# Kernel tuning notes

Measured on AMD Instinct MI355X. Metric: run time of the kernel, lower is better.

Reference implementation:

```python
import jax, jax.numpy as jnp
import numpy as np

N_NODES = 100000
N_EDGES = 1600000
D_IN = 128
D_HID = 128
D_OUT = 64


def setup_inputs() -> dict:
    key = jax.random.key(0)
    ks = jax.random.split(key, 8)
    x = jax.random.normal(ks[0], (N_NODES, D_IN), dtype=jnp.float32)
    edge_index = jax.random.randint(ks[1], (2, N_EDGES), 0, N_NODES, dtype=jnp.int64)
    s1 = 1.0 / np.sqrt(D_IN)
    s2 = 1.0 / np.sqrt(D_HID)
    W1 = jax.random.uniform(ks[2], (D_IN, D_HID), jnp.float32, -s1, s1)
    b1 = jnp.zeros((D_HID,), jnp.float32)
    W2 = jax.random.uniform(ks[3], (D_HID, D_HID), jnp.float32, -s2, s2)
    b2 = jnp.zeros((D_HID,), jnp.float32)
    fc_W = jax.random.uniform(ks[4], (D_HID, D_OUT), jnp.float32, -s2, s2)
    fc_b = jax.random.uniform(ks[5], (D_OUT,), jnp.float32, -s2, s2)
    return {"x": x, "edge_index": edge_index, "W1": W1, "b1": b1,
            "W2": W2, "b2": b2, "fc_W": fc_W, "fc_b": fc_b}


def _gcn_norm(edge_index, n_nodes):
    # add self-loops, compute symmetric normalization D^{-1/2} A D^{-1/2}
    loops = jnp.arange(n_nodes, dtype=edge_index.dtype)
    src = jnp.concatenate([edge_index[0], loops])  # [E+N]
    dst = jnp.concatenate([edge_index[1], loops])
    ones = jnp.ones(src.shape[0], jnp.float32)
    deg = jax.ops.segment_sum(ones, dst, num_segments=n_nodes)  # [N]
    dinv = 1.0 / jnp.sqrt(deg)  # deg >= 1 thanks to self-loops
    norm = dinv[src] * dinv[dst]  # [E+N]
    return src, dst, norm


def _gcn_conv(x, W, b, src, dst, norm, n_nodes):
    h = x @ W                                  # [N, d]
    msg = h[src] * norm[:, None]               # gather + scale, [E+N, d]
    out = jax.ops.segment_sum(msg, dst, num_segments=n_nodes)  # scatter-add
    return out + b


def reference(x, edge_index, W1, b1, W2, b2, fc_W, fc_b):
    n = x.shape[0]
    src, dst, norm = _gcn_norm(edge_index, n)
    h = jax.nn.relu(_gcn_conv(x, W1, b1, src, dst, norm, n))
    # dropout is identity in inference mode
    h = jax.nn.relu(_gcn_conv(h, W2, b2, src, dst, norm, n))
    return h @ fc_W + fc_b
```

## Files before the change

kernel.cpp:

```cpp
#include <hip/hip_runtime.h>

typedef __attribute__((ext_vector_type(8))) short bf16x8;
typedef __attribute__((ext_vector_type(4))) float f32x4;
typedef __attribute__((ext_vector_type(2))) float f32x2;

__device__ __forceinline__ unsigned short f2bf(float x) {
  union { float f; unsigned u; } v; v.f = x;
  return (unsigned short)((v.u + 0x7fffu + ((v.u >> 16) & 1u)) >> 16);
}


__global__ __launch_bounds__(256) void bhist_k(const int* __restrict__ dst,
                                               int* __restrict__ bcnt, int E, int B) {
  __shared__ int h[512];
  for (int i = threadIdx.x; i < B; i += 256) h[i] = 0;
  __syncthreads();
  for (int e = blockIdx.x * 256 + threadIdx.x; e < E; e += gridDim.x * 256)
    atomicAdd(&h[dst[e] >> 8], 1);
  __syncthreads();
  for (int i = threadIdx.x; i < B; i += 256)
    if (h[i]) atomicAdd(&bcnt[i * 16], h[i]);
}

__global__ __launch_bounds__(256) void bin_k(const int* __restrict__ src,
                                             const int* __restrict__ dst,
                                             const int* __restrict__ bcnt,
                                             int* __restrict__ bfill,
                                             unsigned* __restrict__ ebuf, int E, int B) {
  __shared__ int hist[512];
  __shared__ int base[512];
  __shared__ int sd[256];
  int t = threadIdx.x;
  int i0 = 2 * t, i1 = 2 * t + 1;
  int v0 = (i0 < B) ? bcnt[i0 * 16] : 0;
  int v1 = (i1 < B) ? bcnt[i1 * 16] : 0;
  int ts = v0 + v1;
  sd[t] = ts; __syncthreads();
  for (int off = 1; off < 256; off <<= 1) {
    int x = (t >= off) ? sd[t - off] : 0;
    __syncthreads();
    sd[t] += x;
    __syncthreads();
  }
  int excl = sd[t] - ts;
  base[i0] = excl;
  base[i1] = excl + v0;
  __syncthreads();

  int chunk = (E + gridDim.x - 1) / gridDim.x;
  int e0 = blockIdx.x * chunk;
  int e1 = e0 + chunk; if (e1 > E) e1 = E;
  for (int i = t; i < B; i += 256) hist[i] = 0;
  __syncthreads();
  for (int e = e0 + t; e < e1; e += 256) atomicAdd(&hist[dst[e] >> 8], 1);
  __syncthreads();
  for (int i = t; i < B; i += 256) {
    int c = hist[i];
    hist[i] = base[i] + (c ? atomicAdd(&bfill[i * 16], c) : 0);
  }
  __syncthreads();
  for (int e = e0 + t; e < e1; e += 256) {
    int d = dst[e];
    int b = d >> 8;
    int pos = atomicAdd(&hist[b], 1);
    ebuf[pos] = ((unsigned)(d & 255) << 17) | (unsigned)src[e];
  }
}

__global__ __launch_bounds__(256) void bsort_k(const unsigned* __restrict__ ebuf,
                                               const int* __restrict__ bcnt,
                                               int* __restrict__ csr,
                                               int* __restrict__ row_start,
                                               float* __restrict__ dinv, int N, int B, int E) {
  __shared__ int cnt[256];
  __shared__ int sd[256];
  __shared__ int ofs[256];
  __shared__ int sorted[8192];
  __shared__ int s_bs, s_m;
  int b = blockIdx.x, t = threadIdx.x;
  int i0 = 2 * t, i1 = 2 * t + 1;
  int v0 = (i0 < B) ? bcnt[i0 * 16] : 0;
  int v1 = (i1 < B) ? bcnt[i1 * 16] : 0;
  int ts = v0 + v1;
  sd[t] = ts; __syncthreads();
  for (int off = 1; off < 256; off <<= 1) {
    int x = (t >= off) ? sd[t - off] : 0;
    __syncthreads();
    sd[t] += x;
    __syncthreads();
  }
  int excl = sd[t] - ts;
  if (i0 == b) { s_bs = excl; s_m = v0; }
  if (i1 == b) { s_bs = excl + v0; s_m = v1; }
  if (b == 0 && t == 0) row_start[N] = E;
  __syncthreads();
  int bs = s_bs, m = s_m;
  if (m > 8192) m = 8192;

  cnt[t] = 0;
  __syncthreads();
  for (int i = t; i < m; i += 256) atomicAdd(&cnt[ebuf[bs + i] >> 17], 1);
  __syncthreads();
  int deg = cnt[t];
  sd[t] = deg; __syncthreads();
  for (int off = 1; off < 256; off <<= 1) {
    int x = (t >= off) ? sd[t - off] : 0;
    __syncthreads();
    sd[t] += x;
    __syncthreads();
  }
  int nexcl = sd[t] - deg;
  ofs[t] = nexcl;
  int node = (b << 8) + t;
  if (node < N) {
    row_start[node] = bs + nexcl;
    dinv[node] = rsqrtf((float)(deg + 1));
  }
  __syncthreads();
  for (int i = t; i < m; i += 256) {
    unsigned r = ebuf[bs + i];
    int d = r >> 17;
    int p = atomicAdd(&ofs[d], 1);
    if (p < 8192) sorted[p] = (int)(r & 0x1FFFFu);
  }
  __syncthreads();
  for (int i = t; i < m; i += 256) csr[bs + i] = sorted[i];
}

template <int NCOL, bool INF32, bool OUTF32, bool SCALE>
__global__ __launch_bounds__(256) void gemm_k(const void* __restrict__ Ap,
                                              const float* __restrict__ W,
                                              const float* __restrict__ bias,
                                              const float* __restrict__ rowscale,
                                              void* __restrict__ Cp, int M) {
  __shared__ __align__(16) unsigned short Ws[NCOL * 136];
  int tid = threadIdx.x;
  for (int e = tid; e < 128 * NCOL; e += 256) {
    int k = e / NCOL, n = e % NCOL;
    Ws[n * 136 + k] = f2bf(W[e]);
  }
  __syncthreads();

  int wave = tid >> 6, lane = tid & 63;
  int q = lane >> 4, r = lane & 15;
  const int NT = NCOL / 16;
  int ntile = M >> 4;
  for (int tile = blockIdx.x * 4 + wave; tile < ntile; tile += gridDim.x * 4) {
    int row = tile * 16 + r;
    bf16x8 a[4];
    if (INF32) {
      const float* A = (const float*)Ap + (size_t)row * 128 + q * 8;
#pragma unroll
      for (int kk = 0; kk < 4; kk++) {
        const float4* p = (const float4*)(A + kk * 32);
        float4 f0 = p[0], f1 = p[1];
        bf16x8 tt;
        tt[0] = (short)f2bf(f0.x); tt[1] = (short)f2bf(f0.y);
        tt[2] = (short)f2bf(f0.z); tt[3] = (short)f2bf(f0.w);
        tt[4] = (short)f2bf(f1.x); tt[5] = (short)f2bf(f1.y);
        tt[6] = (short)f2bf(f1.z); tt[7] = (short)f2bf(f1.w);
        a[kk] = tt;
      }
    } else {
      const unsigned short* A = (const unsigned short*)Ap + (size_t)row * 128 + q * 8;
#pragma unroll
      for (int kk = 0; kk < 4; kk++) a[kk] = *(const bf16x8*)(A + kk * 32);
    }
    f32x4 acc[NT];
#pragma unroll
    for (int nt = 0; nt < NT; nt++) { acc[nt][0] = 0.f; acc[nt][1] = 0.f; acc[nt][2] = 0.f; acc[nt][3] = 0.f; }
#pragma unroll
    for (int kk = 0; kk < 4; kk++) {
#pragma unroll
      for (int nt = 0; nt < NT; nt++) {
        bf16x8 bfr = *(const bf16x8*)&Ws[(nt * 16 + r) * 136 + kk * 32 + q * 8];
        acc[nt] = __builtin_amdgcn_mfma_f32_16x16x32_bf16(a[kk], bfr, acc[nt], 0, 0, 0);
      }
    }
#pragma unroll
    for (int rr = 0; rr < 4; rr++) {
      int orow = tile * 16 + q * 4 + rr;
      float rs = SCALE ? rowscale[orow] : 1.f;
#pragma unroll
      for (int nt = 0; nt < NT; nt++) {
        int ocol = nt * 16 + r;
        if (OUTF32)
          ((float*)Cp)[(size_t)orow * NCOL + ocol] = acc[nt][rr] + bias[ocol];
        else
          ((unsigned short*)Cp)[(size_t)orow * NCOL + ocol] = f2bf(acc[nt][rr] * rs);
      }
    }
  }
}

__global__ __launch_bounds__(256) void agg_k(const unsigned short* __restrict__ hs,
                                             const float* __restrict__ dinv,
                                             const int* __restrict__ row_start,
                                             const int* __restrict__ csr,
                                             const float* __restrict__ bias,
                                             unsigned short* __restrict__ out, int N) {
  int lane = threadIdx.x & 63;
  int node = (blockIdx.x * 256 + threadIdx.x) >> 6;
  if (node >= N) return;
  int g = lane >> 4, r = lane & 15;
  float di = dinv[node];
  int beg = row_start[node];
  int deg = row_start[node + 1] - beg;

  f32x2 acc2[4];
#pragma unroll
  for (int i = 0; i < 4; i++) { acc2[i][0] = 0.f; acc2[i][1] = 0.f; }

#define ACCADD(U)                                                              \
  {                                                                            \
    f32x2 p;                                                                   \
    p[0] = __uint_as_float((U).x << 16);                                       \
    p[1] = __uint_as_float((U).x & 0xffff0000u); acc2[0] += p;                 \
    p[0] = __uint_as_float((U).y << 16);                                       \
    p[1] = __uint_as_float((U).y & 0xffff0000u); acc2[1] += p;                 \
    p[0] = __uint_as_float((U).z << 16);                                       \
    p[1] = __uint_as_float((U).z & 0xffff0000u); acc2[2] += p;                 \
    p[0] = __uint_as_float((U).w << 16);                                       \
    p[1] = __uint_as_float((U).w & 0xffff0000u); acc2[3] += p;                 \
  }
#define ACCFMA(U, M)                                                           \
  {                                                                            \
    f32x2 w2; w2[0] = (M); w2[1] = (M);                                        \
    f32x2 p;                                                                   \
    p[0] = __uint_as_float((U).x << 16);                                       \
    p[1] = __uint_as_float((U).x & 0xffff0000u); acc2[0] += p * w2;            \
    p[0] = __uint_as_float((U).y << 16);                                       \
    p[1] = __uint_as_float((U).y & 0xffff0000u); acc2[1] += p * w2;            \
    p[0] = __uint_as_float((U).z << 16);                                       \
    p[1] = __uint_as_float((U).z & 0xffff0000u); acc2[2] += p * w2;            \
    p[0] = __uint_as_float((U).w << 16);                                       \
    p[1] = __uint_as_float((U).w & 0xffff0000u); acc2[3] += p * w2;            \
  }

  for (int base = -1; base < deg; base += 64) {
    int idx = base + lane;
    int s = node;
    if (idx >= 0 && idx < deg) s = csr[beg + idx];
    int cntv = deg - base; if (cntv > 64) cntv = 64;
    int j = 0;
    for (; j + 8 <= cntv; j += 8) {
      int s0 = __shfl(s, j + g);
      int s1 = __shfl(s, j + 4 + g);
      uint4 u0 = *(const uint4*)(hs + (size_t)s0 * 128 + r * 8);
      uint4 u1 = *(const uint4*)(hs + (size_t)s1 * 128 + r * 8);
      ACCADD(u0); ACCADD(u1);
    }
    for (; j < cntv; j += 4) {
      int sj = __shfl(s, j + g);
      float mk = (j + g < cntv) ? 1.f : 0.f;
      uint4 u = *(const uint4*)(hs + (size_t)sj * 128 + r * 8);
      ACCFMA(u, mk);
    }
  }
#undef ACCADD
#undef ACCFMA

  float a[8];
#pragma unroll
  for (int d = 0; d < 4; d++) { a[2 * d] = acc2[d][0]; a[2 * d + 1] = acc2[d][1]; }
#pragma unroll
  for (int i = 0; i < 8; i++) {
    a[i] += __shfl_xor(a[i], 16);
    a[i] += __shfl_xor(a[i], 32);
  }

  if (g == 0) {
    bf16x8 t;
#pragma unroll
    for (int i = 0; i < 8; i++) {
      float v = a[i] * di + bias[r * 8 + i];
      if (v < 0.f) v = 0.f;
      t[i] = (short)f2bf(v);
    }
    *(bf16x8*)(out + (size_t)node * 128 + r * 8) = t;
  }
}

extern "C" void kernel_launch(void* const* d_in, const int* in_sizes, int n_in,
                              void* d_out, int out_size, void* d_ws, size_t ws_size,
                              hipStream_t stream) {
  const float* x  = (const float*)d_in[0];
  const int* ei   = (const int*)d_in[1];
  const float* W1 = (const float*)d_in[2];
  const float* b1 = (const float*)d_in[3];
  const float* W2 = (const float*)d_in[4];
  const float* b2 = (const float*)d_in[5];
  const float* fcW = (const float*)d_in[6];
  const float* fcb = (const float*)d_in[7];
  float* out = (float*)d_out;

  int N = in_sizes[0] / 128;
  int E = in_sizes[1] / 2;
  int B = (N + 255) >> 8;
  const int* src = ei;
  const int* dst = ei + E;

  char* w = (char*)d_ws;
  auto alloc = [&](size_t b) { char* p = w; w += (b + 255) & ~(size_t)255; return p; };
  float* dinv      = (float*)alloc((size_t)N * 4);
  int*   row_start = (int*)alloc((size_t)(N + 1) * 4);
  int*   batom     = (int*)alloc((size_t)(B + 1) * 128);
  int*   bcnt      = batom;
  int*   bfill     = batom + (size_t)(B + 1) * 16;
  unsigned* ebuf   = (unsigned*)alloc((size_t)E * 4);
  int*   csr       = (int*)alloc((size_t)E * 4);
  unsigned short* bufA = (unsigned short*)alloc((size_t)N * 128 * 2);
  unsigned short* bufB = (unsigned short*)alloc((size_t)N * 128 * 2);

  hipMemsetAsync(batom, 0, (size_t)(B + 1) * 128, stream);

  bhist_k<<<256, 256, 0, stream>>>(dst, bcnt, E, B);
  bin_k<<<256, 256, 0, stream>>>(src, dst, bcnt, bfill, ebuf, E, B);
  bsort_k<<<B, 256, 0, stream>>>(ebuf, bcnt, csr, row_start, dinv, N, B, E);

  gemm_k<128, true, false, true><<<782, 256, 0, stream>>>((const void*)x, W1, nullptr, dinv,
                                                          (void*)bufA, N);
  agg_k<<<(N + 3) / 4, 256, 0, stream>>>(bufA, dinv, row_start, csr, b1, bufB, N);
  gemm_k<128, false, false, true><<<782, 256, 0, stream>>>((const void*)bufB, W2, nullptr, dinv,
                                                           (void*)bufA, N);
  agg_k<<<(N + 3) / 4, 256, 0, stream>>>(bufA, dinv, row_start, csr, b2, bufB, N);
  gemm_k<64, false, true, false><<<782, 256, 0, stream>>>((const void*)bufB, fcW, fcb, nullptr,
                                                          (void*)out, N);
}
```

Before: 334.7 us.

## Slice hidden features into column slabs so aggregation gathers stay cache-resident

The GEMM epilogue now writes bf16 hidden features in 8 column slabs of 16 features each, laid out slab-major. The aggregation kernel launches 8x the blocks, each block handling one slab, so the gather working set per slab is much smaller and more likely to stay in cache. This trades wider 16-byte gathers per edge for 4-byte gathers, repeats the CSR index reads 8 times, and produces narrower output stores.

```diff
diff --git a/kernel.cpp b/kernel.cpp
--- a/kernel.cpp
+++ b/kernel.cpp
@@ -127,7 +127,7 @@
   for (int i = t; i < m; i += 256) csr[bs + i] = sorted[i];
 }
 
-template <int NCOL, bool INF32, bool OUTF32, bool SCALE>
+template <int NCOL, bool INF32, bool OUTF32>
 __global__ __launch_bounds__(256) void gemm_k(const void* __restrict__ Ap,
                                               const float* __restrict__ W,
                                               const float* __restrict__ bias,
@@ -180,14 +180,16 @@
 #pragma unroll
     for (int rr = 0; rr < 4; rr++) {
       int orow = tile * 16 + q * 4 + rr;
-      float rs = SCALE ? rowscale[orow] : 1.f;
+      float rs = OUTF32 ? 1.f : rowscale[orow];
 #pragma unroll
       for (int nt = 0; nt < NT; nt++) {
-        int ocol = nt * 16 + r;
-        if (OUTF32)
+        if (OUTF32) {
+          int ocol = nt * 16 + r;
           ((float*)Cp)[(size_t)orow * NCOL + ocol] = acc[nt][rr] + bias[ocol];
-        else
-          ((unsigned short*)Cp)[(size_t)orow * NCOL + ocol] = f2bf(acc[nt][rr] * rs);
+        } else {
+          ((unsigned short*)Cp)[(size_t)nt * M * 16 + (size_t)orow * 16 + r] =
+              f2bf(acc[nt][rr] * rs);
+        }
       }
     }
   }
@@ -200,84 +202,64 @@
                                              const float* __restrict__ bias,
                                              unsigned short* __restrict__ out, int N) {
   int lane = threadIdx.x & 63;
-  int node = (blockIdx.x * 256 + threadIdx.x) >> 6;
+  int wave = threadIdx.x >> 6;
+  int s = blockIdx.x & 7;
+  int node = (blockIdx.x >> 3) * 4 + wave;
   if (node >= N) return;
-  int g = lane >> 4, r = lane & 15;
+  int g = lane >> 3, r = lane & 7;
+  const unsigned short* bs_ = hs + (size_t)s * N * 16;
   float di = dinv[node];
   int beg = row_start[node];
   int deg = row_start[node + 1] - beg;
 
-  f32x2 acc2[4];
-#pragma unroll
-  for (int i = 0; i < 4; i++) { acc2[i][0] = 0.f; acc2[i][1] = 0.f; }
-
-#define ACCADD(U)                                                              \
-  {                                                                            \
-    f32x2 p;                                                                   \
-    p[0] = __uint_as_float((U).x << 16);                                       \
-    p[1] = __uint_as_float((U).x & 0xffff0000u); acc2[0] += p;                 \
-    p[0] = __uint_as_float((U).y << 16);                                       \
-    p[1] = __uint_as_float((U).y & 0xffff0000u); acc2[1] += p;                 \
-    p[0] = __uint_as_float((U).z << 16);                                       \
-    p[1] = __uint_as_float((U).z & 0xffff0000u); acc2[2] += p;                 \
-    p[0] = __uint_as_float((U).w << 16);                                       \
-    p[1] = __uint_as_float((U).w & 0xffff0000u); acc2[3] += p;                 \
-  }
-#define ACCFMA(U, M)                                                           \
-  {                                                                            \
-    f32x2 w2; w2[0] = (M); w2[1] = (M);                                        \
-    f32x2 p;                                                                   \
-    p[0] = __uint_as_float((U).x << 16);                                       \
-    p[1] = __uint_as_float((U).x & 0xffff0000u); acc2[0] += p * w2;            \
-    p[0] = __uint_as_float((U).y << 16);                                       \
-    p[1] = __uint_as_float((U).y & 0xffff0000u); acc2[1] += p * w2;            \
-    p[0] = __uint_as_float((U).z << 16);                                       \
-    p[1] = __uint_as_float((U).z & 0xffff0000u); acc2[2] += p * w2;            \
-    p[0] = __uint_as_float((U).w << 16);                                       \
-    p[1] = __uint_as_float((U).w & 0xffff0000u); acc2[3] += p * w2;            \
-  }
+  f32x2 acc; acc[0] = 0.f; acc[1] = 0.f;
+
+#define ACC2(U)                                                                \
+  { f32x2 p; p[0] = __uint_as_float((U) << 16);                                \
+    p[1] = __uint_as_float((U) & 0xffff0000u); acc += p; }
+#define ACC2M(U, MK)                                                           \
+  { f32x2 p, m2; m2[0] = (MK); m2[1] = (MK);                                   \
+    p[0] = __uint_as_float((U) << 16);                                         \
+    p[1] = __uint_as_float((U) & 0xffff0000u); acc += p * m2; }
 
   for (int base = -1; base < deg; base += 64) {
     int idx = base + lane;
-    int s = node;
-    if (idx >= 0 && idx < deg) s = csr[beg + idx];
+    int sj = node;
+    if (idx >= 0 && idx < deg) sj = csr[beg + idx];
     int cntv = deg - base; if (cntv > 64) cntv = 64;
     int j = 0;
-    for (; j + 8 <= cntv; j += 8) {
-      int s0 = __shfl(s, j + g);
-      int s1 = __shfl(s, j + 4 + g);
-      uint4 u0 = *(const uint4*)(hs + (size_t)s0 * 128 + r * 8);
-      uint4 u1 = *(const uint4*)(hs + (size_t)s1 * 128 + r * 8);
-      ACCADD(u0); ACCADD(u1);
-    }
-    for (; j < cntv; j += 4) {
-      int sj = __shfl(s, j + g);
+    for (; j + 32 <= cntv; j += 32) {
+      int e0 = __shfl(sj, j + g);
+      int e1 = __shfl(sj, j + 8 + g);
+      int e2 = __shfl(sj, j + 16 + g);
+      int e3 = __shfl(sj, j + 24 + g);
+      unsigned u0 = *(const unsigned*)(bs_ + (size_t)e0 * 16 + r * 2);
+      unsigned u1 = *(const unsigned*)(bs_ + (size_t)e1 * 16 + r * 2);
+      unsigned u2 = *(const unsigned*)(bs_ + (size_t)e2 * 16 + r * 2);
+      unsigned u3 = *(const unsigned*)(bs_ + (size_t)e3 * 16 + r * 2);
+      ACC2(u0); ACC2(u1); ACC2(u2); ACC2(u3);
+    }
+    for (; j < cntv; j += 8) {
+      int ej = __shfl(sj, j + g);
       float mk = (j + g < cntv) ? 1.f : 0.f;
-      uint4 u = *(const uint4*)(hs + (size_t)sj * 128 + r * 8);
-      ACCFMA(u, mk);
-    }
-  }
-#undef ACCADD
-#undef ACCFMA
-
-  float a[8];
-#pragma unroll
-  for (int d = 0; d < 4; d++) { a[2 * d] = acc2[d][0]; a[2 * d + 1] = acc2[d][1]; }
-#pragma unroll
-  for (int i = 0; i < 8; i++) {
-    a[i] += __shfl_xor(a[i], 16);
-    a[i] += __shfl_xor(a[i], 32);
-  }
+      unsigned u = *(const unsigned*)(bs_ + (size_t)ej * 16 + r * 2);
+      ACC2M(u, mk);
+    }
+  }
+#undef ACC2
+#undef ACC2M
+
+  acc[0] += __shfl_xor(acc[0], 8);  acc[1] += __shfl_xor(acc[1], 8);
+  acc[0] += __shfl_xor(acc[0], 16); acc[1] += __shfl_xor(acc[1], 16);
+  acc[0] += __shfl_xor(acc[0], 32); acc[1] += __shfl_xor(acc[1], 32);
 
   if (g == 0) {
-    bf16x8 t;
-#pragma unroll
-    for (int i = 0; i < 8; i++) {
-      float v = a[i] * di + bias[r * 8 + i];
-      if (v < 0.f) v = 0.f;
-      t[i] = (short)f2bf(v);
-    }
-    *(bf16x8*)(out + (size_t)node * 128 + r * 8) = t;
+    float v0 = acc[0] * di + bias[s * 16 + r * 2];
+    float v1 = acc[1] * di + bias[s * 16 + r * 2 + 1];
+    if (v0 < 0.f) v0 = 0.f;
+    if (v1 < 0.f) v1 = 0.f;
+    unsigned pk = (unsigned)f2bf(v0) | ((unsigned)f2bf(v1) << 16);
+    *(unsigned*)(out + (size_t)node * 128 + s * 16 + r * 2) = pk;
   }
 }
 
@@ -318,12 +300,14 @@
   bin_k<<<256, 256, 0, stream>>>(src, dst, bcnt, bfill, ebuf, E, B);
   bsort_k<<<B, 256, 0, stream>>>(ebuf, bcnt, csr, row_start, dinv, N, B, E);
 
-  gemm_k<128, true, false, true><<<782, 256, 0, stream>>>((const void*)x, W1, nullptr, dinv,
-                                                          (void*)bufA, N);
-  agg_k<<<(N + 3) / 4, 256, 0, stream>>>(bufA, dinv, row_start, csr, b1, bufB, N);
-  gemm_k<128, false, false, true><<<782, 256, 0, stream>>>((const void*)bufB, W2, nullptr, dinv,
-                                                           (void*)bufA, N);
-  agg_k<<<(N + 3) / 4, 256, 0, stream>>>(bufA, dinv, row_start, csr, b2, bufB, N);
-  gemm_k<64, false, true, false><<<782, 256, 0, stream>>>((const void*)bufB, fcW, fcb, nullptr,
-                                                          (void*)out, N);
-}
+  int aggGrid = 8 * ((N + 3) / 4);
+
+  gemm_k<128, true, false><<<782, 256, 0, stream>>>((const void*)x, W1, nullptr, dinv,
+                                                    (void*)bufA, N);
+  agg_k<<<aggGrid, 256, 0, stream>>>(bufA, dinv, row_start, csr, b1, bufB, N);
+  gemm_k<128, false, false><<<782, 256, 0, stream>>>((const void*)bufB, W2, nullptr, dinv,
+                                                     (void*)bufA, N);
+  agg_k<<<aggGrid, 256, 0, stream>>>(bufA, dinv, row_start, csr, b2, bufB, N);
+  gemm_k<64, false, true><<<782, 256, 0, stream>>>((const void*)bufB, fcW, fcb, nullptr,
+                                                   (void*)out, N);
+}
```

New measurement: 671.6 us. 101% more time.
